# Kernel tuning notes

Measured on AMD Instinct MI355X. Metric: run time of the kernel, lower is better.

The kernel has to match this reference:

```python
import jax, jax.numpy as jnp
import numpy as np

LABEL_SIZE = 32
HIDDEN = 1024
TARGET = 1  # args.target
N_EVENTS = 4096
N_SIM = 4096


def setup_inputs() -> dict:
    key = jax.random.key(0)
    ks = jax.random.split(key, 10)
    L, H, n, n_sim = LABEL_SIZE, HIDDEN, N_EVENTS, N_SIM
    label_seq = jax.random.randint(ks[0], (n,), 0, L + 1)
    # strictly increasing event times (positive gaps)
    gaps = jax.random.uniform(ks[1], (n,), minval=0.01, maxval=1.0)
    time_seq = jnp.cumsum(gaps)
    sim_time_idx = jax.random.randint(ks[2], (n_sim,), 0, n - 1)
    sim_time_seq = time_seq[sim_time_idx] + jax.random.uniform(ks[3], (n_sim,), minval=0.0, maxval=0.5)
    stdv = 1.0 / np.sqrt(H)
    u = lambda k, shape: jax.random.uniform(k, shape, minval=-stdv, maxval=stdv)
    Emb = u(ks[4], (H, L + 1))
    W = u(ks[5], (7, H, H))
    U = u(ks[6], (7, H, H))
    d = jnp.zeros((7, H), dtype=jnp.float32)
    w = u(ks[7], (L, H))
    log_s = jnp.zeros((L,), dtype=jnp.float32)
    return {"label_seq": label_seq, "time_seq": time_seq, "sim_time_seq": sim_time_seq,
            "sim_time_idx": sim_time_idx, "ignore_first": 1,
            "Emb": Emb, "W": W, "U": U, "d": d, "w": w, "log_s": log_s}


def _neg_loglik(label_seq, time_seq, sim_time_seq, sim_time_idx, ignore_first,
                Emb, W, U, d, w, log_s):
    H = Emb.shape[0]
    tgt = TARGET
    emb = Emb[:, label_seq].T              # (n, H) event-label embeddings
    # Precompute input-to-gate projections for all steps: W @ label_prev
    Wx = jnp.einsum('ehk,nk->neh', W, emb[:-1])   # (n-1, 7, H)
    dts = time_seq[1:] - time_seq[:-1]            # (n-1,)

    def step(carry, inp):
        c_t, h_t, c_bar = carry
        wx, dt = inp
        temp = wx + jnp.einsum('ehk,k->eh', U, h_t) + d   # (7, H)
        i_g = jax.nn.sigmoid(temp[0])
        f_g = jax.nn.sigmoid(temp[1])
        z = jnp.tanh(temp[2])
        o = jax.nn.sigmoid(temp[3])
        i_b = jax.nn.sigmoid(temp[4])
        f_b = jax.nn.sigmoid(temp[5])
        delta = jax.nn.softplus(temp[6])
        c = f_g * c_t + i_g * z
        c_bar_n = f_b * c_bar + i_b * z
        c_t_n = c_bar_n + (c - c_bar_n) * jnp.exp(-delta * dt)
        h_n = o * jnp.tanh(c_t_n)
        return (c_t_n, h_n, c_bar_n), (h_n, c_bar_n, c, delta, o)

    z0 = jnp.zeros((H,), dtype=time_seq.dtype)
    _, (all_h, all_cbar, all_c, all_delta, all_o) = jax.lax.scan(step, (z0, z0, z0), (Wx, dts))

    def h_to_lambd(h):
        s = jnp.exp(log_s)
        return s * jax.nn.softplus((h @ w.T) / s) + 1e-9

    beg = 1 if ignore_first else 0
    h_evt = all_h[beg:-1]                               # (n-2-beg, H)
    lambd = h_to_lambd(h_evt)                           # (n-2-beg, L)
    mask = label_seq[1 + beg:-1] == tgt
    term1 = jnp.sum(jnp.where(mask, jnp.log(lambd[:, tgt - 1]), 0.0))

    decay = jnp.exp(-all_delta[sim_time_idx] * (sim_time_seq - time_seq[sim_time_idx])[:, None])
    c_sim = all_cbar[sim_time_idx] + (all_c[sim_time_idx] - all_cbar[sim_time_idx]) * decay
    h_sim = all_o[sim_time_idx] * jnp.tanh(c_sim)
    lambd_sim = h_to_lambd(h_sim)
    term2 = jnp.mean(lambd_sim[:, tgt - 1]) * (time_seq[-1] - time_seq[0])
    return -(term1 - term2)


def reference(label_seq, time_seq, sim_time_seq, sim_time_idx, ignore_first, Emb, W, U, d, w, log_s):
    return _neg_loglik(label_seq, time_seq, sim_time_seq, sim_time_idx, ignore_first,
                       Emb, W, U, d, w, log_s)
```

## Files before the change

kernel.cpp:

```cpp
#include <hip/hip_runtime.h>
#include <math.h>

#define H      1024
#define LBLP1  33
#define NE     4096
#define NS     4096
#define NSTEP  (NE - 1)
#define TGT    1
#define NWG    256
#define UPW    4
#define ROWS   28
#define SCAN_THREADS 512
#define LEAF_GROUPS 16
#define ROOT_OFF (LEAF_GROUPS * 32)
#define FLAG_OFF (ROOT_OFF + 32)
#define BAR_UINTS 1024

__device__ __forceinline__ float wave_sum(float v) {
#pragma unroll
    for (int o = 32; o > 0; o >>= 1) v += __shfl_xor(v, o, 64);
    return v;
}

__device__ __forceinline__ float softplusf(float x) {
    return x > 0.f ? x + log1pf(expf(-x)) : log1pf(expf(x));
}
__device__ __forceinline__ float sigmoidf(float x) {
    return 1.f / (1.f + expf(-x));
}

__global__ void wemb_kernel(const float* __restrict__ W, const float* __restrict__ Emb,
                            const float* __restrict__ dbias, float* __restrict__ WEmb) {
    int gw   = blockIdx.x * (blockDim.x >> 6) + (threadIdx.x >> 6);
    int lane = threadIdx.x & 63;
    if (gw >= 7 * H * LBLP1) return;
    int row = gw / LBLP1;
    int l   = gw - row * LBLP1;
    const float* wrow = W + (size_t)row * H;
    float a = 0.f;
#pragma unroll
    for (int m = 0; m < 16; ++m) {
        int k = lane + (m << 6);
        a = fmaf(wrow[k], Emb[k * LBLP1 + l], a);
    }
    a = wave_sum(a);
    if (lane == 0) WEmb[(size_t)row * LBLP1 + l] = a + dbias[row];
}

__global__ __launch_bounds__(SCAN_THREADS)
void scan_kernel(const float* __restrict__ WEmb, const float* __restrict__ U,
                 const int* __restrict__ label_seq, const float* __restrict__ time_seq,
                 float* __restrict__ hbuf, unsigned* __restrict__ bar,
                 float* __restrict__ all_h, float* __restrict__ all_o,
                 float* __restrict__ all_cb, float* __restrict__ all_cc,
                 float* __restrict__ all_dl) {
    const int tid  = threadIdx.x;
    const int wg   = blockIdx.x;
    const int wave = tid >> 6;
    const int lane = tid & 63;

    extern __shared__ float smem[];
    float* Uld    = smem;
    float* h_sh   = Uld + ROWS * H;
    float* act_sh = h_sh + H;

    for (int idx = tid; idx < ROWS * H; idx += SCAN_THREADS) {
        int r = idx >> 10, k = idx & (H - 1);
        int e = r >> 2, j = r & 3;
        Uld[idx] = U[((size_t)e * H + (wg * UPW + j)) * H + k];
    }

    float c_t = 0.f, cbar = 0.f;
    const float4* h4 = (const float4*)h_sh;

    for (int t = 0; t < NSTEP; ++t) {
        const int lab = label_seq[t];
        const float dt = time_seq[t + 1] - time_seq[t];

        unsigned long long hv = 0ull;
        if (t > 0) {
            const unsigned long long* hin =
                (const unsigned long long*)(hbuf + (t & 1) * H);
            hv = __hip_atomic_load(hin + tid, __ATOMIC_RELAXED,
                                   __HIP_MEMORY_SCOPE_AGENT);
        }
        float gb[4];
#pragma unroll
        for (int i = 0; i < 4; ++i) {
            int r = wave + (i << 3);
            if (r < ROWS) {
                int e = r >> 2, j = r & 3;
                gb[i] = WEmb[((size_t)e * H + (wg * UPW + j)) * LBLP1 + lab];
            } else gb[i] = 0.f;
        }

        {
            union { unsigned long long u; float f[2]; } cv; cv.u = hv;
            h_sh[2 * tid]     = cv.f[0];
            h_sh[2 * tid + 1] = cv.f[1];
        }
        __syncthreads();

#pragma unroll
        for (int i = 0; i < 4; ++i) {
            int r = wave + (i << 3);
            if (r < ROWS) {
                const float4* u4 = (const float4*)(Uld + (r << 10));
                float a = 0.f;
#pragma unroll
                for (int m = 0; m < 4; ++m) {
                    float4 u  = u4[(m << 6) + lane];
                    float4 hh = h4[(m << 6) + lane];
                    a = fmaf(u.x, hh.x, a); a = fmaf(u.y, hh.y, a);
                    a = fmaf(u.z, hh.z, a); a = fmaf(u.w, hh.w, a);
                }
                a = wave_sum(a);
                if (lane == 0) {
                    float g = gb[i] + a;
                    int e = r >> 2;
                    float act;
                    if (e == 2)      act = tanhf(g);
                    else if (e == 6) act = softplusf(g);
                    else             act = sigmoidf(g);
                    act_sh[r] = act;
                }
            }
        }
        __syncthreads();

        if (tid < UPW) {
            float i_g = act_sh[tid],      f_g = act_sh[4 + tid];
            float z   = act_sh[8 + tid],  o   = act_sh[12 + tid];
            float i_b = act_sh[16 + tid], f_b = act_sh[20 + tid];
            float dl  = act_sh[24 + tid];
            float c   = fmaf(f_g, c_t, i_g * z);
            float cbn = fmaf(f_b, cbar, i_b * z);
            float ctn = cbn + (c - cbn) * expf(-dl * dt);
            float hn  = o * tanhf(ctn);
            c_t = ctn; cbar = cbn;
            int u = wg * UPW + tid;
            float* hb_out = hbuf + ((t + 1) & 1) * H;
            __hip_atomic_store(&hb_out[u], hn, __ATOMIC_RELAXED,
                               __HIP_MEMORY_SCOPE_AGENT);
            size_t p = (size_t)t * H + u;
            all_h [p] = hn;
            all_o [p] = o;
            all_cb[p] = cbn;
            all_cc[p] = c;
            all_dl[p] = dl;
        }

        if (t + 1 < NSTEP) {
            if (tid == 0) {
                __threadfence_block();
                unsigned old = atomicAdd(&bar[(wg >> 4) * 32], 1u);
                if ((old & 15u) == 15u) {
                    unsigned rold = atomicAdd(&bar[ROOT_OFF], 1u);
                    if ((rold & 15u) == 15u) {
                        __hip_atomic_store(&bar[FLAG_OFF], (unsigned)(t + 1),
                                           __ATOMIC_RELAXED, __HIP_MEMORY_SCOPE_AGENT);
                    }
                }
                while (__hip_atomic_load(&bar[FLAG_OFF], __ATOMIC_RELAXED,
                                         __HIP_MEMORY_SCOPE_AGENT) < (unsigned)(t + 1)) {
                    __builtin_amdgcn_s_sleep(1);
                }
            }
            __syncthreads();
        }
    }
}

__global__ void term1_kernel(const float* __restrict__ all_h, const int* __restrict__ label_seq,
                             const float* __restrict__ w, const float* __restrict__ log_s,
                             const int* __restrict__ ignore_first, float* __restrict__ acc) {
    int beg = (*ignore_first) ? 1 : 0;
    int j = blockIdx.x;
    if (j >= (NSTEP - 1 - beg)) return;
    if (label_seq[1 + beg + j] != TGT) return;
    const float* hrow = all_h + (size_t)(beg + j) * H;
    const float* w0 = w + (TGT - 1) * H;
    float part = 0.f;
    for (int i = threadIdx.x; i < H; i += blockDim.x) part += hrow[i] * w0[i];
    __shared__ float red[4];
    part = wave_sum(part);
    if ((threadIdx.x & 63) == 0) red[threadIdx.x >> 6] = part;
    __syncthreads();
    if (threadIdx.x == 0) {
        float tot = red[0] + red[1] + red[2] + red[3];
        float s0 = expf(log_s[TGT - 1]);
        float lam = s0 * softplusf(tot / s0) + 1e-9f;
        atomicAdd(acc, logf(lam));
    }
}

__global__ void term2_kernel(const float* __restrict__ all_o, const float* __restrict__ all_cb,
                             const float* __restrict__ all_cc, const float* __restrict__ all_dl,
                             const int* __restrict__ sim_idx, const float* __restrict__ sim_time,
                             const float* __restrict__ time_seq, const float* __restrict__ w,
                             const float* __restrict__ log_s, float* __restrict__ acc) {
    int i = blockIdx.x;
    int idx = sim_idx[i];
    float dtp = sim_time[i] - time_seq[idx];
    size_t base = (size_t)idx * H;
    const float* w0 = w + (TGT - 1) * H;
    float part = 0.f;
    for (int hh = threadIdx.x; hh < H; hh += blockDim.x) {
        float cb = all_cb[base + hh];
        float cc = all_cc[base + hh];
        float dl = all_dl[base + hh];
        float oo = all_o [base + hh];
        float cs = cb + (cc - cb) * expf(-dl * dtp);
        part += oo * tanhf(cs) * w0[hh];
    }
    __shared__ float red[4];
    part = wave_sum(part);
    if ((threadIdx.x & 63) == 0) red[threadIdx.x >> 6] = part;
    __syncthreads();
    if (threadIdx.x == 0) {
        float tot = red[0] + red[1] + red[2] + red[3];
        float s0 = expf(log_s[TGT - 1]);
        float lam = s0 * softplusf(tot / s0) + 1e-9f;
        atomicAdd(acc + 1, lam);
    }
}

__global__ void finish_kernel(const float* __restrict__ acc, const float* __restrict__ time_seq,
                              float* __restrict__ out) {
    float T = time_seq[NE - 1] - time_seq[0];
    out[0] = -(acc[0] - acc[1] * (T / (float)NS));
}

extern "C" void kernel_launch(void* const* d_in, const int* in_sizes, int n_in,
                              void* d_out, int out_size, void* d_ws, size_t ws_size,
                              hipStream_t stream) {
    const int*   label_seq    = (const int*)  d_in[0];
    const float* time_seq     = (const float*)d_in[1];
    const float* sim_time     = (const float*)d_in[2];
    const int*   sim_idx      = (const int*)  d_in[3];
    const int*   ignore_first = (const int*)  d_in[4];
    const float* Emb   = (const float*)d_in[5];
    const float* W     = (const float*)d_in[6];
    const float* U     = (const float*)d_in[7];
    const float* dbias = (const float*)d_in[8];
    const float* w     = (const float*)d_in[9];
    const float* log_s = (const float*)d_in[10];
    float* out = (float*)d_out;

    float* ws = (float*)d_ws;
    size_t off = 0;
    unsigned* bar = (unsigned*)ws;  off += BAR_UINTS;
    float* acc    = ws + off;       off += 32;
    float* WEmb   = ws + off;       off += 7 * H * LBLP1;
    off = (off + 3) & ~(size_t)3;
    float* hbuf   = ws + off;       off += 2 * H;
    float* all_h  = ws + off;       off += (size_t)NSTEP * H;
    float* all_o  = ws + off;       off += (size_t)NSTEP * H;
    float* all_cb = ws + off;       off += (size_t)NSTEP * H;
    float* all_cc = ws + off;       off += (size_t)NSTEP * H;
    float* all_dl = ws + off;       off += (size_t)NSTEP * H;

    hipMemsetAsync(bar, 0, BAR_UINTS * sizeof(unsigned), stream);
    hipMemsetAsync(acc, 0, 2 * sizeof(float), stream);

    {
        int total_waves = 7 * H * LBLP1;
        int blocks = (total_waves + 3) / 4;
        hipLaunchKernelGGL(wemb_kernel, dim3(blocks), dim3(256), 0, stream,
                           W, Emb, dbias, WEmb);
    }

    unsigned int smem_bytes = (unsigned int)((ROWS * H + H + ROWS) * sizeof(float));
    hipFuncSetAttribute((const void*)scan_kernel, hipFuncAttributeMaxDynamicSharedMemorySize,
                        (int)smem_bytes);
    void* args[] = { (void*)&WEmb, (void*)&U, (void*)&label_seq, (void*)&time_seq,
                     (void*)&hbuf, (void*)&bar, (void*)&all_h, (void*)&all_o,
                     (void*)&all_cb, (void*)&all_cc, (void*)&all_dl };
    hipLaunchCooperativeKernel((void*)scan_kernel, dim3(NWG), dim3(SCAN_THREADS),
                               args, smem_bytes, stream);

    hipLaunchKernelGGL(term1_kernel, dim3(NSTEP - 1), dim3(256), 0, stream,
                       all_h, label_seq, w, log_s, ignore_first, acc);
    hipLaunchKernelGGL(term2_kernel, dim3(NS), dim3(256), 0, stream,
                       all_o, all_cb, all_cc, all_dl, sim_idx, sim_time, time_seq, w, log_s, acc);
    hipLaunchKernelGGL(finish_kernel, dim3(1), dim3(1), 0, stream, acc, time_seq, out);
}
```

Measured before the change: 19.63 ms.

## Replace grid barrier with sentinel-polled hidden state and cache gate biases

Drops the hierarchical atomic grid barrier. Each workgroup now spins on the previous step's all_h row, which is pre-filled with a 0xFF sentinel, until every value has been written. This removes the per-step barrier round-trip and the double-buffered hbuf. It also preloads the per-workgroup WEmb slice into LDS and restructures the WEmb precompute around a transposed Emb so its loads coalesce. The cost is a memset of all_h, and correctness now depends on a NaN bit pattern never being a real h value.

```diff
diff --git a/kernel.cpp b/kernel.cpp
--- a/kernel.cpp
+++ b/kernel.cpp
@@ -11,10 +11,7 @@
 #define UPW    4
 #define ROWS   28
 #define SCAN_THREADS 512
-#define LEAF_GROUPS 16
-#define ROOT_OFF (LEAF_GROUPS * 32)
-#define FLAG_OFF (ROOT_OFF + 32)
-#define BAR_UINTS 1024
+#define SENTINEL 0xFFFFFFFFu
 
 __device__ __forceinline__ float wave_sum(float v) {
 #pragma unroll
@@ -29,28 +26,37 @@
     return 1.f / (1.f + expf(-x));
 }
 
-__global__ void wemb_kernel(const float* __restrict__ W, const float* __restrict__ Emb,
+__global__ void embT_kernel(const float* __restrict__ Emb, float* __restrict__ EmbT) {
+    int l = blockIdx.x;
+    for (int k = threadIdx.x; k < H; k += blockDim.x)
+        EmbT[(size_t)l * H + k] = Emb[(size_t)k * LBLP1 + l];
+}
+
+__global__ void wemb_kernel(const float* __restrict__ W, const float* __restrict__ EmbT,
                             const float* __restrict__ dbias, float* __restrict__ WEmb) {
-    int gw   = blockIdx.x * (blockDim.x >> 6) + (threadIdx.x >> 6);
+    int row  = blockIdx.x;
+    int wave = threadIdx.x >> 6;
     int lane = threadIdx.x & 63;
-    if (gw >= 7 * H * LBLP1) return;
-    int row = gw / LBLP1;
-    int l   = gw - row * LBLP1;
-    const float* wrow = W + (size_t)row * H;
-    float a = 0.f;
-#pragma unroll
-    for (int m = 0; m < 16; ++m) {
-        int k = lane + (m << 6);
-        a = fmaf(wrow[k], Emb[k * LBLP1 + l], a);
-    }
-    a = wave_sum(a);
-    if (lane == 0) WEmb[(size_t)row * LBLP1 + l] = a + dbias[row];
+    __shared__ float wrow[H];
+    for (int i = threadIdx.x; i < H; i += blockDim.x) wrow[i] = W[(size_t)row * H + i];
+    __syncthreads();
+    float db = dbias[row];
+    for (int l = wave; l < LBLP1; l += 4) {
+        const float* ec = EmbT + (size_t)l * H;
+        float a = 0.f;
+#pragma unroll
+        for (int m = 0; m < 16; ++m) {
+            int k = lane + (m << 6);
+            a = fmaf(wrow[k], ec[k], a);
+        }
+        a = wave_sum(a);
+        if (lane == 0) WEmb[(size_t)row * LBLP1 + l] = a + db;
+    }
 }
 
 __global__ __launch_bounds__(SCAN_THREADS)
 void scan_kernel(const float* __restrict__ WEmb, const float* __restrict__ U,
                  const int* __restrict__ label_seq, const float* __restrict__ time_seq,
-                 float* __restrict__ hbuf, unsigned* __restrict__ bar,
                  float* __restrict__ all_h, float* __restrict__ all_o,
                  float* __restrict__ all_cb, float* __restrict__ all_cc,
                  float* __restrict__ all_dl) {
@@ -63,43 +69,50 @@
     float* Uld    = smem;
     float* h_sh   = Uld + ROWS * H;
     float* act_sh = h_sh + H;
+    float* wes    = act_sh + 32;
 
     for (int idx = tid; idx < ROWS * H; idx += SCAN_THREADS) {
         int r = idx >> 10, k = idx & (H - 1);
         int e = r >> 2, j = r & 3;
         Uld[idx] = U[((size_t)e * H + (wg * UPW + j)) * H + k];
     }
+    for (int idx = tid; idx < ROWS * LBLP1; idx += SCAN_THREADS) {
+        int r = idx / LBLP1, l = idx - r * LBLP1;
+        int e = r >> 2, j = r & 3;
+        wes[idx] = WEmb[((size_t)e * H + (wg * UPW + j)) * LBLP1 + l];
+    }
 
     float c_t = 0.f, cbar = 0.f;
     const float4* h4 = (const float4*)h_sh;
 
     for (int t = 0; t < NSTEP; ++t) {
-        const int lab = label_seq[t];
-        const float dt = time_seq[t + 1] - time_seq[t];
-
-        unsigned long long hv = 0ull;
-        if (t > 0) {
-            const unsigned long long* hin =
-                (const unsigned long long*)(hbuf + (t & 1) * H);
-            hv = __hip_atomic_load(hin + tid, __ATOMIC_RELAXED,
-                                   __HIP_MEMORY_SCOPE_AGENT);
-        }
-        float gb[4];
-#pragma unroll
-        for (int i = 0; i < 4; ++i) {
-            int r = wave + (i << 3);
-            if (r < ROWS) {
-                int e = r >> 2, j = r & 3;
-                gb[i] = WEmb[((size_t)e * H + (wg * UPW + j)) * LBLP1 + lab];
-            } else gb[i] = 0.f;
-        }
-
-        {
-            union { unsigned long long u; float f[2]; } cv; cv.u = hv;
-            h_sh[2 * tid]     = cv.f[0];
-            h_sh[2 * tid + 1] = cv.f[1];
+        const int   lab = label_seq[t];
+        const float dt  = time_seq[t + 1] - time_seq[t];
+
+        if (tid < 256) {
+            float4 hv;
+            if (t > 0) {
+                const unsigned* src = (const unsigned*)(all_h + (size_t)(t - 1) * H) + (tid << 2);
+                unsigned v0, v1, v2, v3;
+                do {
+                    v0 = __hip_atomic_load(src + 0, __ATOMIC_RELAXED, __HIP_MEMORY_SCOPE_AGENT);
+                    v1 = __hip_atomic_load(src + 1, __ATOMIC_RELAXED, __HIP_MEMORY_SCOPE_AGENT);
+                    v2 = __hip_atomic_load(src + 2, __ATOMIC_RELAXED, __HIP_MEMORY_SCOPE_AGENT);
+                    v3 = __hip_atomic_load(src + 3, __ATOMIC_RELAXED, __HIP_MEMORY_SCOPE_AGENT);
+                } while (v0 == SENTINEL || v1 == SENTINEL || v2 == SENTINEL || v3 == SENTINEL);
+                union { unsigned u[4]; float4 f; } cv;
+                cv.u[0] = v0; cv.u[1] = v1; cv.u[2] = v2; cv.u[3] = v3;
+                hv = cv.f;
+            } else {
+                hv = make_float4(0.f, 0.f, 0.f, 0.f);
+            }
+            ((float4*)h_sh)[tid] = hv;
         }
         __syncthreads();
+
+        float4 hr[4];
+#pragma unroll
+        for (int m = 0; m < 4; ++m) hr[m] = h4[(m << 6) + lane];
 
 #pragma unroll
         for (int i = 0; i < 4; ++i) {
@@ -109,14 +122,13 @@
                 float a = 0.f;
 #pragma unroll
                 for (int m = 0; m < 4; ++m) {
-                    float4 u  = u4[(m << 6) + lane];
-                    float4 hh = h4[(m << 6) + lane];
-                    a = fmaf(u.x, hh.x, a); a = fmaf(u.y, hh.y, a);
-                    a = fmaf(u.z, hh.z, a); a = fmaf(u.w, hh.w, a);
+                    float4 u = u4[(m << 6) + lane];
+                    a = fmaf(u.x, hr[m].x, a); a = fmaf(u.y, hr[m].y, a);
+                    a = fmaf(u.z, hr[m].z, a); a = fmaf(u.w, hr[m].w, a);
                 }
                 a = wave_sum(a);
                 if (lane == 0) {
-                    float g = gb[i] + a;
+                    float g = wes[r * LBLP1 + lab] + a;
                     int e = r >> 2;
                     float act;
                     if (e == 2)      act = tanhf(g);
@@ -138,35 +150,12 @@
             float ctn = cbn + (c - cbn) * expf(-dl * dt);
             float hn  = o * tanhf(ctn);
             c_t = ctn; cbar = cbn;
-            int u = wg * UPW + tid;
-            float* hb_out = hbuf + ((t + 1) & 1) * H;
-            __hip_atomic_store(&hb_out[u], hn, __ATOMIC_RELAXED,
-                               __HIP_MEMORY_SCOPE_AGENT);
-            size_t p = (size_t)t * H + u;
-            all_h [p] = hn;
+            size_t p = (size_t)t * H + wg * UPW + tid;
+            __hip_atomic_store(&all_h[p], hn, __ATOMIC_RELAXED, __HIP_MEMORY_SCOPE_AGENT);
             all_o [p] = o;
             all_cb[p] = cbn;
             all_cc[p] = c;
             all_dl[p] = dl;
-        }
-
-        if (t + 1 < NSTEP) {
-            if (tid == 0) {
-                __threadfence_block();
-                unsigned old = atomicAdd(&bar[(wg >> 4) * 32], 1u);
-                if ((old & 15u) == 15u) {
-                    unsigned rold = atomicAdd(&bar[ROOT_OFF], 1u);
-                    if ((rold & 15u) == 15u) {
-                        __hip_atomic_store(&bar[FLAG_OFF], (unsigned)(t + 1),
-                                           __ATOMIC_RELAXED, __HIP_MEMORY_SCOPE_AGENT);
-                    }
-                }
-                while (__hip_atomic_load(&bar[FLAG_OFF], __ATOMIC_RELAXED,
-                                         __HIP_MEMORY_SCOPE_AGENT) < (unsigned)(t + 1)) {
-                    __builtin_amdgcn_s_sleep(1);
-                }
-            }
-            __syncthreads();
         }
     }
 }
@@ -249,33 +238,29 @@
 
     float* ws = (float*)d_ws;
     size_t off = 0;
-    unsigned* bar = (unsigned*)ws;  off += BAR_UINTS;
-    float* acc    = ws + off;       off += 32;
-    float* WEmb   = ws + off;       off += 7 * H * LBLP1;
+    float* acc    = ws + off;  off += 32;
+    float* EmbT   = ws + off;  off += (size_t)LBLP1 * H;
+    float* WEmb   = ws + off;  off += 7 * H * LBLP1;
     off = (off + 3) & ~(size_t)3;
-    float* hbuf   = ws + off;       off += 2 * H;
-    float* all_h  = ws + off;       off += (size_t)NSTEP * H;
-    float* all_o  = ws + off;       off += (size_t)NSTEP * H;
-    float* all_cb = ws + off;       off += (size_t)NSTEP * H;
-    float* all_cc = ws + off;       off += (size_t)NSTEP * H;
-    float* all_dl = ws + off;       off += (size_t)NSTEP * H;
-
-    hipMemsetAsync(bar, 0, BAR_UINTS * sizeof(unsigned), stream);
+    float* all_h  = ws + off;  off += (size_t)NSTEP * H;
+    float* all_o  = ws + off;  off += (size_t)NSTEP * H;
+    float* all_cb = ws + off;  off += (size_t)NSTEP * H;
+    float* all_cc = ws + off;  off += (size_t)NSTEP * H;
+    float* all_dl = ws + off;  off += (size_t)NSTEP * H;
+
     hipMemsetAsync(acc, 0, 2 * sizeof(float), stream);
-
-    {
-        int total_waves = 7 * H * LBLP1;
-        int blocks = (total_waves + 3) / 4;
-        hipLaunchKernelGGL(wemb_kernel, dim3(blocks), dim3(256), 0, stream,
-                           W, Emb, dbias, WEmb);
-    }
-
-    unsigned int smem_bytes = (unsigned int)((ROWS * H + H + ROWS) * sizeof(float));
+    hipMemsetAsync(all_h, 0xFF, (size_t)NSTEP * H * sizeof(float), stream);
+
+    hipLaunchKernelGGL(embT_kernel, dim3(LBLP1), dim3(256), 0, stream, Emb, EmbT);
+    hipLaunchKernelGGL(wemb_kernel, dim3(7 * H), dim3(256), 0, stream,
+                       W, EmbT, dbias, WEmb);
+
+    unsigned int smem_bytes = (unsigned int)((ROWS * H + H + 32 + ROWS * LBLP1) * sizeof(float));
     hipFuncSetAttribute((const void*)scan_kernel, hipFuncAttributeMaxDynamicSharedMemorySize,
                         (int)smem_bytes);
     void* args[] = { (void*)&WEmb, (void*)&U, (void*)&label_seq, (void*)&time_seq,
-                     (void*)&hbuf, (void*)&bar, (void*)&all_h, (void*)&all_o,
-                     (void*)&all_cb, (void*)&all_cc, (void*)&all_dl };
+                     (void*)&all_h, (void*)&all_o, (void*)&all_cb, (void*)&all_cc,
+                     (void*)&all_dl };
     hipLaunchCooperativeKernel((void*)scan_kernel, dim3(NWG), dim3(SCAN_THREADS),
                                args, smem_bytes, stream);
 
```

Result: no change. 19.71 ms (+0.4%).
